# Optimization experiments

Measured on AMD Instinct MI355X. Metric: run time of the kernel, lower is better.

## Reference

```python
import jax, jax.numpy as jnp
import numpy as np

N_GAUSS, FEAT = 2048, 128
H, W = 128, 128
FX, FY = 128.0, 128.0
CX, CY = W / 2.0, H / 2.0
MAX_STEP = 0.05          # xyz_offset_max_step
CLIP_SCALING = 0.2       # clip_scaling
LOW_PASS = 0.3           # 2D covariance dilation (as in reference CUDA rasterizer)


def _quat_to_rot(q):
    # q: [N,4] normalized, (w,x,y,z) convention (rotation bias init has 1 at index 0)
    w, x, y, z = q[:, 0], q[:, 1], q[:, 2], q[:, 3]
    R = jnp.stack([
        1 - 2 * (y * y + z * z), 2 * (x * y - w * z), 2 * (x * z + w * y),
        2 * (x * y + w * z), 1 - 2 * (x * x + z * z), 2 * (y * z - w * x),
        2 * (x * z - w * y), 2 * (y * z + w * x), 1 - 2 * (x * x + y * y),
    ], axis=-1)
    return R.reshape(-1, 3, 3)


def setup_inputs() -> dict:
    key = jax.random.key(0)
    ks = jax.random.split(key, 8)
    s = 0.02
    x = jax.random.normal(ks[0], (N_GAUSS, FEAT), jnp.float32)
    pts = jax.random.normal(ks[1], (N_GAUSS, 3), jnp.float32) * 0.4
    # camera 2.5 units in front of the point cloud, looking down +z (view z = z + 2.5)
    viewmat = jnp.asarray(np.array(
        [[1, 0, 0, 0], [0, 1, 0, 0], [0, 0, 1, 2.5], [0, 0, 0, 1]], dtype=np.float32))
    w_shs = jax.random.normal(ks[2], (3, FEAT), jnp.float32) * s
    b_shs = jnp.zeros((3,), jnp.float32)
    w_scale = jax.random.normal(ks[3], (3, FEAT), jnp.float32) * s
    b_scale = jnp.full((3,), -3.0, jnp.float32)              # init_scaling
    w_xyz = jax.random.normal(ks[4], (3, FEAT), jnp.float32) * s
    b_xyz = jnp.zeros((3,), jnp.float32)
    w_opac = jax.random.normal(ks[5], (1, FEAT), jnp.float32) * s
    b_opac = jnp.full((1,), -2.1972246, jnp.float32)         # inverse_sigmoid(0.1)
    w_rot = jax.random.normal(ks[6], (4, FEAT), jnp.float32) * s
    b_rot = jnp.array([1.0, 0.0, 0.0, 0.0], jnp.float32)
    return dict(x=x, pts=pts, viewmat=viewmat, w_shs=w_shs, b_shs=b_shs,
                w_scale=w_scale, b_scale=b_scale, w_xyz=w_xyz, b_xyz=b_xyz,
                w_opac=w_opac, b_opac=b_opac, w_rot=w_rot, b_rot=b_rot)


def _forward(x, pts, viewmat, w_shs, b_shs, w_scale, b_scale, w_xyz, b_xyz,
             w_opac, b_opac, w_rot, b_rot):
    # ---- GSLayer decode (use_rgb=True path) ----
    rgb = jax.nn.sigmoid(x @ w_shs.T + b_shs)                     # [N,3]
    scale = jnp.clip(jnp.exp(x @ w_scale.T + b_scale), 0.0, CLIP_SCALING)
    offset = (jax.nn.sigmoid(x @ w_xyz.T + b_xyz) - 0.5) * MAX_STEP
    xyz = pts + offset                                            # [N,3]
    opac = jax.nn.sigmoid(x @ w_opac.T + b_opac)                  # [N,1]
    q = x @ w_rot.T + b_rot
    q = q / jnp.linalg.norm(q, axis=-1, keepdims=True)
    R = _quat_to_rot(q)                                           # [N,3,3]
    cov3d = jnp.einsum('nij,nj,nkj->nik', R, scale * scale, R)    # R S^2 R^T

    # ---- projection (EWA splatting) ----
    Rv, tv = viewmat[:3, :3], viewmat[:3, 3]
    p = xyz @ Rv.T + tv                                           # view space [N,3]
    tx, ty = p[:, 0], p[:, 1]
    tz = jnp.maximum(p[:, 2], 1e-3)
    u = FX * tx / tz + CX
    v = FY * ty / tz + CY
    zr = jnp.zeros_like(tz)
    J = jnp.stack([
        jnp.stack([FX / tz, zr, -FX * tx / (tz * tz)], axis=-1),
        jnp.stack([zr, FY / tz, -FY * ty / (tz * tz)], axis=-1),
    ], axis=1)                                                    # [N,2,3]
    M = jnp.einsum('nij,jk->nik', J, Rv)                          # [N,2,3]
    C2 = jnp.einsum('nij,njk,nlk->nil', M, cov3d, M)              # [N,2,2]
    a = C2[:, 0, 0] + LOW_PASS
    b = C2[:, 0, 1]
    c = C2[:, 1, 1] + LOW_PASS
    det = a * c - b * b + 1e-12
    cA, cB, cC = c / det, -b / det, a / det                       # conic

    # ---- per-pixel gaussian eval ----
    px = jnp.arange(W, dtype=jnp.float32) + 0.5
    py = jnp.arange(H, dtype=jnp.float32) + 0.5
    gx = jnp.tile(px, H)                                          # [P]
    gy = jnp.repeat(py, W)                                        # [P]
    dx = gx[None, :] - u[:, None]                                 # [N,P]
    dy = gy[None, :] - v[:, None]
    power = -0.5 * (cA[:, None] * dx * dx + cC[:, None] * dy * dy) - cB[:, None] * dx * dy
    power = jnp.minimum(power, 0.0)
    alpha = jnp.minimum(0.99, opac * jnp.exp(power))              # [N,P]
    vis = (p[:, 2] > 0.01).astype(alpha.dtype)[:, None]           # znear cull
    alpha = alpha * vis
    alpha = jnp.where(alpha < 1.0 / 255.0, 0.0, alpha)

    # ---- depth-sorted alpha compositing ----
    order = jnp.argsort(tz)
    alpha_s = alpha[order]
    rgb_s = rgb[order]
    T = jnp.cumprod(1.0 - alpha_s, axis=0)
    T_excl = jnp.concatenate([jnp.ones_like(T[:1]), T[:-1]], axis=0)
    wgt = alpha_s * T_excl                                        # [N,P]
    img = jnp.einsum('np,nc->pc', wgt, rgb_s).reshape(H, W, 3)
    return img


def reference(x, pts, viewmat, w_shs, b_shs, w_scale, b_scale, w_xyz, b_xyz,
              w_opac, b_opac, w_rot, b_rot):
    return _forward(x, pts, viewmat, w_shs, b_shs, w_scale, b_scale,
                    w_xyz, b_xyz, w_opac, b_opac, w_rot, b_rot)
```

## Files before the change

kernel.cpp:

```cpp
#include <hip/hip_runtime.h>
#include <math.h>

#define NG 2048
#define FEATN 128
#define NBLK 256
#define LOG2E 1.4426950408889634f
#define MAGIC1 0x7F3DC0DEu
#define MAGIC2 0x6B42F00Du

typedef unsigned long long u64;

#define RB_BYTE   32768
#define RC_BYTE   65536
#define KEY_BYTE  98304
#define SORT_BYTE 131072
#define F1_BYTE   229376
#define F2_BYTE   230400

__device__ __forceinline__ float sigmoidf_(float z) { return 1.0f / (1.0f + expf(-z)); }

__device__ __forceinline__ void stg8(void* p, u64 v) {
    __hip_atomic_store((u64*)p, v, __ATOMIC_RELAXED, __HIP_MEMORY_SCOPE_AGENT);
}
__device__ __forceinline__ u64 ldg8(const void* p) {
    return __hip_atomic_load((const u64*)p, __ATOMIC_RELAXED, __HIP_MEMORY_SCOPE_AGENT);
}
__device__ __forceinline__ void stg4(unsigned* p, unsigned v) {
    __hip_atomic_store(p, v, __ATOMIC_RELAXED, __HIP_MEMORY_SCOPE_AGENT);
}
__device__ __forceinline__ unsigned ldg4(const unsigned* p) {
    return __hip_atomic_load(p, __ATOMIC_RELAXED, __HIP_MEMORY_SCOPE_AGENT);
}
__device__ __forceinline__ void st_f4(void* p, float4 v) {
    union { float2 f; u64 u; } a, b;
    a.f = make_float2(v.x, v.y); b.f = make_float2(v.z, v.w);
    stg8(p, a.u); stg8((char*)p + 8, b.u);
}
__device__ __forceinline__ float4 ld_f4(const void* p) {
    union { u64 u; float2 f; } a, b;
    a.u = ldg8(p); b.u = ldg8((const char*)p + 8);
    return make_float4(a.f.x, a.f.y, b.f.x, b.f.y);
}

__global__ __launch_bounds__(1024) void k_fused(
    const float* __restrict__ x, const float* __restrict__ pts, const float* __restrict__ vm,
    const float* __restrict__ w_shs, const float* __restrict__ b_shs,
    const float* __restrict__ w_scale, const float* __restrict__ b_scale,
    const float* __restrict__ w_xyz, const float* __restrict__ b_xyz,
    const float* __restrict__ w_opac, const float* __restrict__ b_opac,
    const float* __restrict__ w_rot, const float* __restrict__ b_rot,
    float* __restrict__ ws, float* __restrict__ out)
{
    __shared__ __attribute__((aligned(16))) char smem_u[512 * 12 * 4];
    __shared__ unsigned short sidx16[NG];
    __shared__ float partT[16][64], partR[16][64], partG[16][64], partB[16][64];
    __shared__ int s_cnt[16];

    float* sw = (float*)smem_u;
    float (*accs)[14] = (float(*)[14])(smem_u + 7168);
    u64* skey = (u64*)smem_u;
    float (*params_lds)[12] = (float(*)[12])smem_u;

    const int tid = threadIdx.x;
    const int wid = tid >> 6, lane = tid & 63;
    const int bid = blockIdx.x;
    char* wsb = (char*)ws;
    u64* keyg = (u64*)(wsb + KEY_BYTE);
    unsigned* flag1 = (unsigned*)(wsb + F1_BYTE);
    unsigned* flag2 = (unsigned*)(wsb + F2_BYTE);
    u64 lmask = (1ull << lane) - 1ull;

    for (int i = tid; i < 14 * FEATN; i += 1024) {
        int r = i >> 7, c0 = i & 127;
        float v;
        if (r < 3)       v = w_shs[r * FEATN + c0];
        else if (r < 6)  v = w_scale[(r - 3) * FEATN + c0];
        else if (r < 9)  v = w_xyz[(r - 6) * FEATN + c0];
        else if (r == 9) v = w_opac[c0];
        else             v = w_rot[(r - 10) * FEATN + c0];
        sw[i] = v;
    }
    __syncthreads();
    {
        int gi = tid >> 7;
        int head = (tid >> 3) & 15;
        int sub = tid & 7;
        int g = bid * 8 + gi;
        if (head < 14) {
            const float4* xp = (const float4*)(x + (size_t)g * FEATN + sub * 16);
            const float* wp = sw + head * FEATN + sub * 16;
            float acc = 0.0f;
#pragma unroll
            for (int k4 = 0; k4 < 4; k4++) {
                float4 xv = xp[k4];
                acc += xv.x * wp[k4 * 4 + 0] + xv.y * wp[k4 * 4 + 1]
                     + xv.z * wp[k4 * 4 + 2] + xv.w * wp[k4 * 4 + 3];
            }
            acc += __shfl_xor(acc, 1);
            acc += __shfl_xor(acc, 2);
            acc += __shfl_xor(acc, 4);
            if (sub == 0) accs[gi][head] = acc;
        }
    }
    __syncthreads();
    if (tid < 8) {
        int g = bid * 8 + tid;
        float acc[14];
#pragma unroll
        for (int j = 0; j < 14; j++) acc[j] = accs[tid][j];

        float r0 = sigmoidf_(acc[0] + b_shs[0]);
        float r1 = sigmoidf_(acc[1] + b_shs[1]);
        float r2 = sigmoidf_(acc[2] + b_shs[2]);
        float s0 = fminf(expf(acc[3] + b_scale[0]), 0.2f);
        float s1 = fminf(expf(acc[4] + b_scale[1]), 0.2f);
        float s2 = fminf(expf(acc[5] + b_scale[2]), 0.2f);
        float o0 = (sigmoidf_(acc[6] + b_xyz[0]) - 0.5f) * 0.05f;
        float o1 = (sigmoidf_(acc[7] + b_xyz[1]) - 0.5f) * 0.05f;
        float o2 = (sigmoidf_(acc[8] + b_xyz[2]) - 0.5f) * 0.05f;
        float opac = sigmoidf_(acc[9] + b_opac[0]);
        float qw = acc[10] + b_rot[0];
        float qx = acc[11] + b_rot[1];
        float qy = acc[12] + b_rot[2];
        float qz = acc[13] + b_rot[3];
        float qn = sqrtf(qw * qw + qx * qx + qy * qy + qz * qz);
        qw /= qn; qx /= qn; qy /= qn; qz /= qn;

        float R[3][3];
        R[0][0] = 1.f - 2.f * (qy * qy + qz * qz);
        R[0][1] = 2.f * (qx * qy - qw * qz);
        R[0][2] = 2.f * (qx * qz + qw * qy);
        R[1][0] = 2.f * (qx * qy + qw * qz);
        R[1][1] = 1.f - 2.f * (qx * qx + qz * qz);
        R[1][2] = 2.f * (qy * qz - qw * qx);
        R[2][0] = 2.f * (qx * qz - qw * qy);
        R[2][1] = 2.f * (qy * qz + qw * qx);
        R[2][2] = 1.f - 2.f * (qx * qx + qy * qy);

        float sq[3] = { s0 * s0, s1 * s1, s2 * s2 };
        float cov[3][3];
#pragma unroll
        for (int i = 0; i < 3; i++)
#pragma unroll
            for (int k = 0; k < 3; k++)
                cov[i][k] = R[i][0] * sq[0] * R[k][0] + R[i][1] * sq[1] * R[k][1] + R[i][2] * sq[2] * R[k][2];

        float Rv[3][3], tv[3];
#pragma unroll
        for (int i = 0; i < 3; i++) {
#pragma unroll
            for (int j = 0; j < 3; j++) Rv[i][j] = vm[i * 4 + j];
            tv[i] = vm[i * 4 + 3];
        }
        float X0 = pts[g * 3 + 0] + o0;
        float X1 = pts[g * 3 + 1] + o1;
        float X2 = pts[g * 3 + 2] + o2;
        float p0 = Rv[0][0] * X0 + Rv[0][1] * X1 + Rv[0][2] * X2 + tv[0];
        float p1 = Rv[1][0] * X0 + Rv[1][1] * X1 + Rv[1][2] * X2 + tv[1];
        float p2 = Rv[2][0] * X0 + Rv[2][1] * X1 + Rv[2][2] * X2 + tv[2];
        float tz = fmaxf(p2, 0.001f);
        float u = 128.0f * p0 / tz + 64.0f;
        float v = 128.0f * p1 / tz + 64.0f;

        float j00 = 128.0f / tz, j02 = -128.0f * p0 / (tz * tz);
        float j11 = 128.0f / tz, j12 = -128.0f * p1 / (tz * tz);
        float M0[3], M1[3];
#pragma unroll
        for (int k = 0; k < 3; k++) {
            M0[k] = j00 * Rv[0][k] + j02 * Rv[2][k];
            M1[k] = j11 * Rv[1][k] + j12 * Rv[2][k];
        }
        float t0[3], t1[3];
#pragma unroll
        for (int k = 0; k < 3; k++) {
            t0[k] = M0[0] * cov[0][k] + M0[1] * cov[1][k] + M0[2] * cov[2][k];
            t1[k] = M1[0] * cov[0][k] + M1[1] * cov[1][k] + M1[2] * cov[2][k];
        }
        float A = t0[0] * M0[0] + t0[1] * M0[1] + t0[2] * M0[2] + 0.3f;
        float B = t0[0] * M1[0] + t0[1] * M1[1] + t0[2] * M1[2];
        float C = t1[0] * M1[0] + t1[1] * M1[1] + t1[2] * M1[2] + 0.3f;
        float det = A * C - B * B + 1e-12f;
        float cA = C / det, cB = -B / det, cC = A / det;

        if (p2 <= 0.01f) opac = 0.0f;

        float rx, ry;
        if (opac >= 1.0f / 255.0f) {
            float L = 2.0f * logf(255.0f * opac);
            rx = sqrtf(L * A) + 0.5f;
            ry = sqrtf(L * C) + 0.5f;
        } else {
            rx = -1e9f; ry = -1e9f;
        }

        st_f4(wsb + (size_t)g * 16,            make_float4(u, v, rx, ry));
        st_f4(wsb + RB_BYTE + (size_t)g * 16,  make_float4(-0.5f * LOG2E * cA, -LOG2E * cB, -0.5f * LOG2E * cC, opac));
        st_f4(wsb + RC_BYTE + (size_t)g * 16,  make_float4(r0, r1, r2, 0.0f));
        stg8(&keyg[g], ((u64)__float_as_uint(tz) << 32) | (unsigned)g);
    }

    asm volatile("s_waitcnt vmcnt(0)" ::: "memory");
    __syncthreads();
    if (tid == 0) stg4(&flag1[bid], MAGIC1);
    {
        int slot = tid & 255;
        while (ldg4(&flag1[slot]) != MAGIC1) __builtin_amdgcn_s_sleep(4);
    }
    __syncthreads();

    skey[tid] = ldg8(&keyg[tid]);
    skey[tid + 1024] = ldg8(&keyg[tid + 1024]);
    __syncthreads();
    if (wid < 8) {
        int g = bid * 8 + wid;
        u64 mk = skey[g];
        const ulonglong2* p2 = (const ulonglong2*)skey;
        int cnt = 0;
#pragma unroll
        for (int q = 0; q < 16; ++q) {
            ulonglong2 two = p2[lane + (q << 6)];
            cnt += (two.x < mk) ? 1 : 0;
            cnt += (two.y < mk) ? 1 : 0;
        }
        cnt += __shfl_xor(cnt, 1);
        cnt += __shfl_xor(cnt, 2);
        cnt += __shfl_xor(cnt, 4);
        cnt += __shfl_xor(cnt, 8);
        cnt += __shfl_xor(cnt, 16);
        cnt += __shfl_xor(cnt, 32);
        if (lane < 6) {
            const char* src = wsb + (lane >> 1) * 32768 + (size_t)g * 16 + (lane & 1) * 8;
            char* dst = wsb + SORT_BYTE + (lane >> 1) * 32768 + (size_t)cnt * 16 + (lane & 1) * 8;
            stg8(dst, ldg8(src));
        }
    }

    asm volatile("s_waitcnt vmcnt(0)" ::: "memory");
    __syncthreads();
    if (tid == 0) stg4(&flag2[bid], MAGIC2);
    {
        int slot = tid & 255;
        while (ldg4(&flag2[slot]) != MAGIC2) __builtin_amdgcn_s_sleep(4);
    }
    __syncthreads();

    const char* SAb = wsb + SORT_BYTE;
    int tx0 = (bid & 15) << 3, ty0 = (bid >> 4) << 3;
    float x0 = tx0 + 0.5f, x1 = tx0 + 7.5f;
    float y0 = ty0 + 0.5f, y1 = ty0 + 7.5f;

    int n = 0;
#pragma unroll
    for (int r = 0; r < 2; ++r) {
        int s = r * 1024 + tid;
        float4 a = ld_f4(SAb + (size_t)s * 16);
        bool keep = (a.x + a.z >= x0) && (a.x - a.z <= x1) &&
                    (a.y + a.w >= y0) && (a.y - a.w <= y1);
        u64 m = __ballot(keep);
        if (lane == 0) s_cnt[wid] = __popcll(m);
        __syncthreads();
        int base = n, total = 0;
#pragma unroll
        for (int w = 0; w < 16; w++) {
            if (w < wid) base += s_cnt[w];
            total += s_cnt[w];
        }
        if (keep) sidx16[base + __popcll(m & lmask)] = (unsigned short)s;
        n += total;
        __syncthreads();
    }

    float gx = x0 + (float)(lane & 7);
    float gy = y0 + (float)(lane >> 3);
    float crT = 1.0f, crR = 0.0f, crG = 0.0f, crB = 0.0f;
    for (int c0 = 0; c0 < n; c0 += 512) {
        int m = min(512, n - c0);
        if (tid < m) {
            int s = sidx16[c0 + tid];
            float4 a = ld_f4(SAb + (size_t)s * 16);
            float4 b = ld_f4(SAb + 32768 + (size_t)s * 16);
            float4 c = ld_f4(SAb + 65536 + (size_t)s * 16);
            float* e = params_lds[tid];
            ((float4*)e)[0] = make_float4(a.x, a.y, b.x, b.y);
            ((float4*)e)[1] = make_float4(b.z, b.w, c.x, c.y);
            e[8] = c.z;
        }
        __syncthreads();

        int seg = (m + 15) >> 4;
        int sb = wid * seg;
        int se = min(m, sb + seg);
        float T = 1.0f, oR = 0.0f, oG = 0.0f, oB = 0.0f;
        for (int i = sb; i < se; ++i) {
            const float* e = params_lds[i];
            float4 e0 = ((const float4*)e)[0];
            float4 e1 = ((const float4*)e)[1];
            float bl = e[8];
            float dx = gx - e0.x, dy = gy - e0.y;
            float pw = dx * (e0.z * dx + e0.w * dy) + e1.x * dy * dy;
            pw = fminf(pw, 0.0f);
            float al = fminf(0.99f, e1.y * exp2f(pw));
            al = (al < 1.0f / 255.0f) ? 0.0f : al;
            float w = al * T;
            oR += w * e1.z;
            oG += w * e1.w;
            oB += w * bl;
            T -= al * T;
        }
        partT[wid][lane] = T;
        partR[wid][lane] = oR;
        partG[wid][lane] = oG;
        partB[wid][lane] = oB;
        __syncthreads();

        if (wid == 0) {
#pragma unroll
            for (int w = 0; w < 16; w++) {
                crR += crT * partR[w][lane];
                crG += crT * partG[w][lane];
                crB += crT * partB[w][lane];
                crT *= partT[w][lane];
            }
        }
        __syncthreads();
    }

    if (wid == 0) {
        int p = (ty0 + (lane >> 3)) * 128 + tx0 + (lane & 7);
        out[p * 3 + 0] = crR;
        out[p * 3 + 1] = crG;
        out[p * 3 + 2] = crB;
    }
}

extern "C" void kernel_launch(void* const* d_in, const int* in_sizes, int n_in,
                              void* d_out, int out_size, void* d_ws, size_t ws_size,
                              hipStream_t stream)
{
    const float* x       = (const float*)d_in[0];
    const float* pts     = (const float*)d_in[1];
    const float* viewmat = (const float*)d_in[2];
    const float* w_shs   = (const float*)d_in[3];
    const float* b_shs   = (const float*)d_in[4];
    const float* w_scale = (const float*)d_in[5];
    const float* b_scale = (const float*)d_in[6];
    const float* w_xyz   = (const float*)d_in[7];
    const float* b_xyz   = (const float*)d_in[8];
    const float* w_opac  = (const float*)d_in[9];
    const float* b_opac  = (const float*)d_in[10];
    const float* w_rot   = (const float*)d_in[11];
    const float* b_rot   = (const float*)d_in[12];
    float* ws = (float*)d_ws;
    float* out = (float*)d_out;

    k_fused<<<NBLK, 1024, 0, stream>>>(x, pts, viewmat, w_shs, b_shs, w_scale, b_scale,
                                       w_xyz, b_xyz, w_opac, b_opac, w_rot, b_rot, ws, out);
}
```

Baseline: 26.64 us.

## Shrink sort keys to 32-bit, poll flags with fewer threads, terminate saturated tiles early

```diff
diff --git a/kernel.cpp b/kernel.cpp
--- a/kernel.cpp
+++ b/kernel.cpp
@@ -55,17 +55,18 @@
     __shared__ unsigned short sidx16[NG];
     __shared__ float partT[16][64], partR[16][64], partG[16][64], partB[16][64];
     __shared__ int s_cnt[16];
+    __shared__ int s_break;
 
     float* sw = (float*)smem_u;
     float (*accs)[14] = (float(*)[14])(smem_u + 7168);
-    u64* skey = (u64*)smem_u;
+    unsigned* skey32 = (unsigned*)smem_u;
     float (*params_lds)[12] = (float(*)[12])smem_u;
 
     const int tid = threadIdx.x;
     const int wid = tid >> 6, lane = tid & 63;
     const int bid = blockIdx.x;
     char* wsb = (char*)ws;
-    u64* keyg = (u64*)(wsb + KEY_BYTE);
+    unsigned* keyg = (unsigned*)(wsb + KEY_BYTE);
     unsigned* flag1 = (unsigned*)(wsb + F1_BYTE);
     unsigned* flag2 = (unsigned*)(wsb + F2_BYTE);
     u64 lmask = (1ull << lane) - 1ull;
@@ -196,31 +197,33 @@
         st_f4(wsb + (size_t)g * 16,            make_float4(u, v, rx, ry));
         st_f4(wsb + RB_BYTE + (size_t)g * 16,  make_float4(-0.5f * LOG2E * cA, -LOG2E * cB, -0.5f * LOG2E * cC, opac));
         st_f4(wsb + RC_BYTE + (size_t)g * 16,  make_float4(r0, r1, r2, 0.0f));
-        stg8(&keyg[g], ((u64)__float_as_uint(tz) << 32) | (unsigned)g);
+        stg4(&keyg[g], __float_as_uint(tz));
     }
 
     asm volatile("s_waitcnt vmcnt(0)" ::: "memory");
     __syncthreads();
     if (tid == 0) stg4(&flag1[bid], MAGIC1);
-    {
-        int slot = tid & 255;
-        while (ldg4(&flag1[slot]) != MAGIC1) __builtin_amdgcn_s_sleep(4);
-    }
-    __syncthreads();
-
-    skey[tid] = ldg8(&keyg[tid]);
-    skey[tid + 1024] = ldg8(&keyg[tid + 1024]);
+    if (tid < 256) {
+        while (ldg4(&flag1[tid]) != MAGIC1) __builtin_amdgcn_s_sleep(4);
+    }
+    __syncthreads();
+
+    ((u64*)skey32)[tid] = ldg8(&((u64*)keyg)[tid]);
     __syncthreads();
     if (wid < 8) {
         int g = bid * 8 + wid;
-        u64 mk = skey[g];
-        const ulonglong2* p2 = (const ulonglong2*)skey;
+        unsigned mk = skey32[g];
+        const uint4* p4 = (const uint4*)skey32;
         int cnt = 0;
 #pragma unroll
-        for (int q = 0; q < 16; ++q) {
-            ulonglong2 two = p2[lane + (q << 6)];
-            cnt += (two.x < mk) ? 1 : 0;
-            cnt += (two.y < mk) ? 1 : 0;
+        for (int q = 0; q < 8; ++q) {
+            int jb = lane + (q << 6);
+            uint4 kv = p4[jb];
+            int j0 = jb << 2;
+            cnt += (kv.x < mk || (kv.x == mk && (j0 + 0) < g)) ? 1 : 0;
+            cnt += (kv.y < mk || (kv.y == mk && (j0 + 1) < g)) ? 1 : 0;
+            cnt += (kv.z < mk || (kv.z == mk && (j0 + 2) < g)) ? 1 : 0;
+            cnt += (kv.w < mk || (kv.w == mk && (j0 + 3) < g)) ? 1 : 0;
         }
         cnt += __shfl_xor(cnt, 1);
         cnt += __shfl_xor(cnt, 2);
@@ -238,9 +241,8 @@
     asm volatile("s_waitcnt vmcnt(0)" ::: "memory");
     __syncthreads();
     if (tid == 0) stg4(&flag2[bid], MAGIC2);
-    {
-        int slot = tid & 255;
-        while (ldg4(&flag2[slot]) != MAGIC2) __builtin_amdgcn_s_sleep(4);
+    if (tid < 256) {
+        while (ldg4(&flag2[tid]) != MAGIC2) __builtin_amdgcn_s_sleep(4);
     }
     __syncthreads();
 
@@ -321,8 +323,11 @@
                 crB += crT * partB[w][lane];
                 crT *= partT[w][lane];
             }
-        }
-        __syncthreads();
+            u64 alive = __ballot(crT >= 1.5e-5f);
+            if (lane == 0) s_break = (alive == 0ull);
+        }
+        __syncthreads();
+        if (s_break) break;
     }
 
     if (wid == 0) {
```

Result: faster. 26.00 us (-2.4%).
